# Performance work log

Hardware: AMD Instinct MI355X
Metric: run time of the kernel (lower is better)

The kernel has to match this reference:

```python
import jax, jax.numpy as jnp
import numpy as np

NUM_HEADS = 12


def setup_inputs() -> dict:
    key = jax.random.key(0)
    ks = jax.random.split(key, 10)
    B, N, C = 8, 1024, 768
    H = NUM_HEADS
    return {
        "x": jax.random.normal(ks[0], (B, N, C), dtype=jnp.float32),
        "geometric": jax.random.uniform(ks[1], (B, 1, 1, 1), dtype=jnp.float32),
        "text": jax.random.uniform(ks[2], (B, 1, 1, 1), dtype=jnp.float32),
        "color": jax.random.uniform(ks[3], (B, 1, 1, 1), dtype=jnp.float32),
        "W_qkv": jax.random.normal(ks[4], (C, 3 * C), dtype=jnp.float32) * 0.02,
        "W_proj": jax.random.normal(ks[5], (C, C), dtype=jnp.float32) * 0.02,
        "b_proj": jax.random.normal(ks[6], (C,), dtype=jnp.float32) * 0.02,
        "geo_bias": jax.random.normal(ks[7], (1, H, 1, 1), dtype=jnp.float32) * 0.1,
        "txt_bias": jax.random.normal(ks[8], (1, H, 1, 1), dtype=jnp.float32) * 0.1,
        "col_bias": jax.random.normal(ks[9], (1, H, 1, 1), dtype=jnp.float32) * 0.1,
    }


def reference(x, geometric, text, color, W_qkv, W_proj, b_proj, geo_bias, txt_bias, col_bias):
    B, N, C = x.shape
    H = NUM_HEADS
    Dh = C // H
    scale = Dh ** -0.5
    # qkv: [B, N, 3, H, Dh] -> q,k,v each [B, H, N, Dh]
    qkv = (x @ W_qkv).reshape(B, N, 3, H, Dh)
    q = jnp.transpose(qkv[:, :, 0], (0, 2, 1, 3))
    k = jnp.transpose(qkv[:, :, 1], (0, 2, 1, 3))
    v = jnp.transpose(qkv[:, :, 2], (0, 2, 1, 3))
    # scores [B, H, N, N] with additive per-head logo biases
    attn = jnp.einsum("bhnd,bhmd->bhnm", q, k) * scale
    attn = attn + geo_bias * geometric + txt_bias * text + col_bias * color
    attn = jax.nn.softmax(attn, axis=-1)
    out = jnp.einsum("bhnm,bhmd->bhnd", attn, v)  # [B, H, N, Dh]
    out = jnp.transpose(out, (0, 2, 1, 3)).reshape(B, N, C)
    return out @ W_proj + b_proj
```

## Files before the change

### kernel.cpp

```cpp
#include <hip/hip_runtime.h>
#include <hip/hip_bf16.h>


typedef __bf16 b16x8 __attribute__((ext_vector_type(8)));
typedef float f32x4 __attribute__((ext_vector_type(4)));

__device__ __forceinline__ ushort f2b(float f) {
    union { float f; uint u; } v; v.f = f;
    uint u = v.u;
    u += 0x7fffu + ((u >> 16) & 1u);
    return (ushort)(u >> 16);
}

__device__ __forceinline__ uint packbf(float a, float b) {
    union { float f; uint u; } ua, ub; ua.f = a; ub.f = b;
    return ((ua.u + 0x8000u) >> 16) | ((ub.u + 0x8000u) & 0xffff0000u);
}

__device__ __forceinline__ void async_cp16(const void* g, void* l) {
    __builtin_amdgcn_global_load_lds(
        (const __attribute__((address_space(1))) unsigned int*)g,
        (__attribute__((address_space(3))) unsigned int*)l, 16, 0, 0);
}


__global__ __launch_bounds__(256)
void k_prep(const float* __restrict__ x, ushort* __restrict__ xb,
            const float* __restrict__ Wqkv, ushort* __restrict__ wqkvt,
            const float* __restrict__ Wproj, ushort* __restrict__ wprojt) {
    __shared__ ushort T[64][65];
    const int blk = blockIdx.x;
    const int t   = threadIdx.x;

    if (blk < 6144) {
        const int i = blk * 256 + t;
        const float4 v = reinterpret_cast<const float4*>(x)[i];
        ushort4 o;
        o.x = f2b(v.x); o.y = f2b(v.y); o.z = f2b(v.z); o.w = f2b(v.w);
        reinterpret_cast<ushort4*>(xb)[i] = o;
        return;
    }

    const bool isqkv = (blk < 6576);
    const int idx = isqkv ? (blk - 6144) : (blk - 6576);
    const int Nin = isqkv ? 2304 : 768;
    const float* W  = isqkv ? Wqkv : Wproj;
    ushort* Wt      = isqkv ? wqkvt : wprojt;
    const int k0 = (idx % 12) * 64;
    const int n0 = (idx / 12) * 64;
    const int r  = t >> 4, cg = (t & 15) * 4;
    #pragma unroll
    for (int rr = 0; rr < 64; rr += 16) {
        const float4 v = *reinterpret_cast<const float4*>(&W[(size_t)(k0 + r + rr) * Nin + n0 + cg]);
        T[r + rr][cg + 0] = f2b(v.x); T[r + rr][cg + 1] = f2b(v.y);
        T[r + rr][cg + 2] = f2b(v.z); T[r + rr][cg + 3] = f2b(v.w);
    }
    __syncthreads();
    #pragma unroll
    for (int rr = 0; rr < 64; rr += 16) {
        ushort4 o;
        o.x = T[cg + 0][r + rr]; o.y = T[cg + 1][r + rr];
        o.z = T[cg + 2][r + rr]; o.w = T[cg + 3][r + rr];
        *reinterpret_cast<ushort4*>(&Wt[(size_t)(n0 + r + rr) * 768 + k0 + cg]) = o;
    }
}


template<int MODE>
__global__ __launch_bounds__(256, 4)
void k_gemm(const ushort* __restrict__ A, const ushort* __restrict__ Bt,
            ushort* __restrict__ qo, ushort* __restrict__ ko, ushort* __restrict__ vo,
            float* __restrict__ co, const float* __restrict__ bias,
            int M, int N, int K) {
    __shared__ ushort As[2][128 * 32];
    __shared__ ushort Bs[2][128 * 32];
    const int id   = blockIdx.x;
    const int xcd  = id & 7;
    const int s    = id >> 3;
    const int by   = xcd * 8 + (s & 7);
    const int bx   = s >> 3;
    const int tid  = threadIdx.x;
    const int lane = tid & 63;
    const int w    = tid >> 6;
    const int wm   = w >> 1, wn = w & 1;
    const int m16  = lane & 15, quad = lane >> 4;
    const int mbase = by * 128, nbase = bx * 128;

    f32x4 acc[4][4];
    #pragma unroll
    for (int i = 0; i < 4; i++)
        #pragma unroll
        for (int j = 0; j < 4; j++) acc[i][j] = (f32x4){0.f, 0.f, 0.f, 0.f};

    const int rS = w * 32 + (lane >> 2);
    const int cS = (lane & 3) * 8;
    const int wOff0 = (w * 2 + 0) * 512;
    const int wOff1 = (w * 2 + 1) * 512;
    const ushort* gA0 = &A [(size_t)(mbase + rS)      * K + cS];
    const ushort* gA1 = &A [(size_t)(mbase + rS + 16) * K + cS];
    const ushort* gB0 = &Bt[(size_t)(nbase + rS)      * K + cS];
    const ushort* gB1 = &Bt[(size_t)(nbase + rS + 16) * K + cS];

    async_cp16(gA0, &As[0][wOff0]);
    async_cp16(gA1, &As[0][wOff1]);
    async_cp16(gB0, &Bs[0][wOff0]);
    async_cp16(gB1, &Bs[0][wOff1]);

    for (int kt = 0; kt < K; kt += 32) {
        const int cur = (kt >> 5) & 1, nxt = cur ^ 1;
        __syncthreads();
        if (kt + 32 < K) {
            async_cp16(gA0 + kt + 32, &As[nxt][wOff0]);
            async_cp16(gA1 + kt + 32, &As[nxt][wOff1]);
            async_cp16(gB0 + kt + 32, &Bs[nxt][wOff0]);
            async_cp16(gB1 + kt + 32, &Bs[nxt][wOff1]);
        }

        b16x8 af[4], bf[4];
        #pragma unroll
        for (int i = 0; i < 4; i++)
            af[i] = *reinterpret_cast<const b16x8*>(&As[cur][(wm * 64 + i * 16 + m16) * 32 + quad * 8]);
        #pragma unroll
        for (int j = 0; j < 4; j++)
            bf[j] = *reinterpret_cast<const b16x8*>(&Bs[cur][(wn * 64 + j * 16 + m16) * 32 + quad * 8]);
        #pragma unroll
        for (int i = 0; i < 4; i++)
            #pragma unroll
            for (int j = 0; j < 4; j++)
                acc[i][j] = __builtin_amdgcn_mfma_f32_16x16x32_bf16(bf[j], af[i], acc[i][j], 0, 0, 0);
    }

    #pragma unroll
    for (int j = 0; j < 4; j++) {
        const int f0 = nbase + wn * 64 + j * 16 + quad * 4;
        #pragma unroll
        for (int i = 0; i < 4; i++) {
            const int tok = mbase + wm * 64 + i * 16 + m16;
            const int b = tok >> 10, n = tok & 1023;
            if (MODE == 0) {
                const int sp  = f0 / 768;
                const int rem = f0 - sp * 768;
                const int h   = rem >> 6;
                const int d0  = rem & 63;
                if (sp < 2) {
                    ushort4 pk;
                    pk.x = f2b(acc[i][j][0]); pk.y = f2b(acc[i][j][1]);
                    pk.z = f2b(acc[i][j][2]); pk.w = f2b(acc[i][j][3]);
                    ushort* base = (sp == 0) ? qo : ko;
                    *reinterpret_cast<ushort4*>(
                        &base[((size_t)(b * 12 + h) * 1024 + n) * 64 + d0]) = pk;
                } else {
                    #pragma unroll
                    for (int r = 0; r < 4; r++)
                        vo[((size_t)(b * 12 + h) * 64 + d0 + r) * 1024 + n] =
                            f2b(acc[i][j][r]);
                }
            } else {
                float4 val;
                val.x = acc[i][j][0] + bias[f0 + 0];
                val.y = acc[i][j][1] + bias[f0 + 1];
                val.z = acc[i][j][2] + bias[f0 + 2];
                val.w = acc[i][j][3] + bias[f0 + 3];
                *reinterpret_cast<float4*>(&co[(size_t)tok * N + f0]) = val;
            }
        }
    }
}


#define AP 72

__global__ __launch_bounds__(256)
void k_attn(const ushort* __restrict__ qa, const ushort* __restrict__ ka,
            const ushort* __restrict__ vt, ushort* __restrict__ ao) {
    __shared__ ushort Ks[64 * AP];
    __shared__ ushort Vs[64 * AP];

    const int l    = blockIdx.x;
    const int xcd  = l & 7;
    const int g    = l >> 3;
    const int head = (g % 12) * 8 + xcd;
    const int qsup = g / 12;
    const int tid  = threadIdx.x;
    const int w    = tid >> 6;
    const int lane = tid & 63;
    const int n    = lane & 15;
    const int q    = lane >> 4;

    const ushort* qh = qa + (size_t)head * 65536;
    const ushort* kh = ka + (size_t)head * 65536;
    const ushort* vh = vt + (size_t)head * 65536;
    const int qrow0 = qsup * 128 + w * 32;

    b16x8 bq0[2], bq1[2];
    #pragma unroll
    for (int u = 0; u < 2; u++) {
        bq0[u] = *reinterpret_cast<const b16x8*>(&qh[(qrow0 + u * 16 + n) * 64 + q * 8]);
        bq1[u] = *reinterpret_cast<const b16x8*>(&qh[(qrow0 + u * 16 + n) * 64 + 32 + q * 8]);
    }

    const int kr0 = tid >> 3, kc0 = (tid & 7) * 8;
    const int kr1 = kr0 + 32, kc1 = kc0;

    int4 kg0, kg1, vg0, vg1;
    kg0 = *reinterpret_cast<const int4*>(&kh[(0 + kr0) * 64 + kc0]);
    kg1 = *reinterpret_cast<const int4*>(&kh[(0 + kr1) * 64 + kc1]);
    vg0 = *reinterpret_cast<const int4*>(&vh[kr0 * 1024 + 0 + kc0]);
    vg1 = *reinterpret_cast<const int4*>(&vh[kr1 * 1024 + 0 + kc1]);

    f32x4 o[2][4];
    #pragma unroll
    for (int u = 0; u < 2; u++)
        #pragma unroll
        for (int dt = 0; dt < 4; dt++) o[u][dt] = (f32x4){0, 0, 0, 0};
    float Lacc[2] = {0.f, 0.f};

    const float SC = 0.125f * 1.4426950408889634f;
    const int s0 = ((q & 1) * 2) * 16 + n;
    const int s1 = s0 + 16;
    const bool lowq = (q < 2);

    for (int m0 = 0; m0 < 1024; m0 += 64) {
        *reinterpret_cast<int4*>(&Ks[kr0 * AP + kc0]) = kg0;
        *reinterpret_cast<int4*>(&Ks[kr1 * AP + kc1]) = kg1;
        *reinterpret_cast<int4*>(&Vs[kr0 * AP + kc0]) = vg0;
        *reinterpret_cast<int4*>(&Vs[kr1 * AP + kc1]) = vg1;
        __syncthreads();

        if (m0 + 64 < 1024) {
            kg0 = *reinterpret_cast<const int4*>(&kh[(m0 + 64 + kr0) * 64 + kc0]);
            kg1 = *reinterpret_cast<const int4*>(&kh[(m0 + 64 + kr1) * 64 + kc1]);
            vg0 = *reinterpret_cast<const int4*>(&vh[kr0 * 1024 + m0 + 64 + kc0]);
            vg1 = *reinterpret_cast<const int4*>(&vh[kr1 * 1024 + m0 + 64 + kc1]);
        }

        #pragma unroll
        for (int mc = 0; mc < 2; mc++) {
            b16x8 ka0t[2], ka1t[2];
            #pragma unroll
            for (int t = 0; t < 2; t++) {
                ka0t[t] = *reinterpret_cast<const b16x8*>(&Ks[(mc * 32 + t * 16 + n) * AP + q * 8]);
                ka1t[t] = *reinterpret_cast<const b16x8*>(&Ks[(mc * 32 + t * 16 + n) * AP + 32 + q * 8]);
            }
            f32x4 st[2][2];
            #pragma unroll
            for (int u = 0; u < 2; u++)
                #pragma unroll
                for (int t = 0; t < 2; t++) {
                    st[u][t] = (f32x4){0, 0, 0, 0};
                    st[u][t] = __builtin_amdgcn_mfma_f32_16x16x32_bf16(ka0t[t], bq0[u], st[u][t], 0, 0, 0);
                    st[u][t] = __builtin_amdgcn_mfma_f32_16x16x32_bf16(ka1t[t], bq1[u], st[u][t], 0, 0, 0);
                }

            union { uint4 u4; b16x8 v; } bp[2];
            #pragma unroll
            for (int u = 0; u < 2; u++) {
                float p00 = __builtin_amdgcn_exp2f(st[u][0][0] * SC);
                float p01 = __builtin_amdgcn_exp2f(st[u][0][1] * SC);
                float p02 = __builtin_amdgcn_exp2f(st[u][0][2] * SC);
                float p03 = __builtin_amdgcn_exp2f(st[u][0][3] * SC);
                float p10 = __builtin_amdgcn_exp2f(st[u][1][0] * SC);
                float p11 = __builtin_amdgcn_exp2f(st[u][1][1] * SC);
                float p12 = __builtin_amdgcn_exp2f(st[u][1][2] * SC);
                float p13 = __builtin_amdgcn_exp2f(st[u][1][3] * SC);
                Lacc[u] += ((p00 + p01) + (p02 + p03)) + ((p10 + p11) + (p12 + p13));

                const uint pk00 = packbf(p00, p01), pk01 = packbf(p02, p03);
                const uint pk10 = packbf(p10, p11), pk11 = packbf(p12, p13);

                uint a, b, dw0, dw1, dw2, dw3;
                a = __shfl((int)pk00, s0); b = __shfl((int)pk10, s0); dw0 = lowq ? a : b;
                a = __shfl((int)pk01, s0); b = __shfl((int)pk11, s0); dw1 = lowq ? a : b;
                a = __shfl((int)pk00, s1); b = __shfl((int)pk10, s1); dw2 = lowq ? a : b;
                a = __shfl((int)pk01, s1); b = __shfl((int)pk11, s1); dw3 = lowq ? a : b;
                bp[u].u4 = (uint4){dw0, dw1, dw2, dw3};
            }

            #pragma unroll
            for (int dt = 0; dt < 4; dt++) {
                const b16x8 av = *reinterpret_cast<const b16x8*>(
                    &Vs[(dt * 16 + n) * AP + mc * 32 + q * 8]);
                #pragma unroll
                for (int u = 0; u < 2; u++)
                    o[u][dt] = __builtin_amdgcn_mfma_f32_16x16x32_bf16(av, bp[u].v, o[u][dt], 0, 0, 0);
            }
        }
        __syncthreads();
    }

    const int bb = head / 12, h = head - bb * 12;
    #pragma unroll
    for (int u = 0; u < 2; u++) {
        float L = Lacc[u];
        L += __shfl_xor(L, 16);
        L += __shfl_xor(L, 32);
        const float inv = 1.f / L;
        ushort* dst = ao + ((size_t)(bb * 1024 + qrow0 + u * 16 + n)) * 768 + h * 64 + q * 4;
        #pragma unroll
        for (int dt = 0; dt < 4; dt++) {
            ushort4 pk;
            pk.x = f2b(o[u][dt][0] * inv);
            pk.y = f2b(o[u][dt][1] * inv);
            pk.z = f2b(o[u][dt][2] * inv);
            pk.w = f2b(o[u][dt][3] * inv);
            *reinterpret_cast<ushort4*>(dst + dt * 16) = pk;
        }
    }
}


extern "C" void kernel_launch(void* const* d_in, const int* in_sizes, int n_in,
                              void* d_out, int out_size, void* d_ws, size_t ws_size,
                              hipStream_t stream) {
    (void)in_sizes; (void)n_in; (void)out_size; (void)ws_size;
    const float* x     = (const float*)d_in[0];
    const float* Wqkv  = (const float*)d_in[4];
    const float* Wproj = (const float*)d_in[5];
    const float* bproj = (const float*)d_in[6];
    float* out = (float*)d_out;

    char* ws = (char*)d_ws;
    ushort* xb     = (ushort*)ws; ws += (size_t)8192 * 768 * 2;
    ushort* wqkvt  = (ushort*)ws; ws += (size_t)2304 * 768 * 2;
    ushort* wprojt = (ushort*)ws; ws += (size_t)768  * 768 * 2;
    ushort* qa     = (ushort*)ws; ws += (size_t)96 * 1024 * 64 * 2;
    ushort* ka     = (ushort*)ws; ws += (size_t)96 * 1024 * 64 * 2;
    ushort* vt     = (ushort*)ws; ws += (size_t)96 * 64 * 1024 * 2;
    ushort* ao     = (ushort*)ws; ws += (size_t)8192 * 768 * 2;

    k_prep<<<dim3(6720), dim3(256), 0, stream>>>(x, xb, Wqkv, wqkvt, Wproj, wprojt);
    k_gemm<0><<<dim3(1152), dim3(256), 0, stream>>>(xb, wqkvt, qa, ka, vt,
                                                    nullptr, nullptr, 8192, 2304, 768);
    k_attn<<<dim3(768), dim3(256), 0, stream>>>(qa, ka, vt, ao);
    k_gemm<1><<<dim3(384), dim3(256), 0, stream>>>(ao, wprojt, nullptr, nullptr, nullptr,
                                                   out, bproj, 8192, 768, 768);
}
```

Baseline: 212.6 us.

## Triple-buffer GEMM K-loop and write V transposed via swapped MFMA operands

Moves the GEMM main loop from double to triple buffering with async global-to-LDS copies. Explicit vmcnt waits let two tiles stay in flight while one is consumed, and the loop now needs only one barrier per step. For V-projection blocks the MFMA operands are swapped, so each lane holds 4 consecutive tokens and can write the transposed V output as packed ushort4 stores instead of scattered 2-byte stores. The larger LDS footprint lowers the launch bound to 3 blocks per CU, which reduces occupancy.

```diff
diff --git a/kernel.cpp b/kernel.cpp
--- a/kernel.cpp
+++ b/kernel.cpp
@@ -67,13 +67,13 @@
 
 
 template<int MODE>
-__global__ __launch_bounds__(256, 4)
+__global__ __launch_bounds__(256, 3)
 void k_gemm(const ushort* __restrict__ A, const ushort* __restrict__ Bt,
             ushort* __restrict__ qo, ushort* __restrict__ ko, ushort* __restrict__ vo,
             float* __restrict__ co, const float* __restrict__ bias,
             int M, int N, int K) {
-    __shared__ ushort As[2][128 * 32];
-    __shared__ ushort Bs[2][128 * 32];
+    __shared__ ushort As[3][128 * 32];
+    __shared__ ushort Bs[3][128 * 32];
     const int id   = blockIdx.x;
     const int xcd  = id & 7;
     const int s    = id >> 3;
@@ -85,6 +85,7 @@
     const int wm   = w >> 1, wn = w & 1;
     const int m16  = lane & 15, quad = lane >> 4;
     const int mbase = by * 128, nbase = bx * 128;
+    const bool vblk = (MODE == 0) && (nbase >= 1536);
 
     f32x4 acc[4][4];
     #pragma unroll
@@ -105,15 +106,22 @@
     async_cp16(gA1, &As[0][wOff1]);
     async_cp16(gB0, &Bs[0][wOff0]);
     async_cp16(gB1, &Bs[0][wOff1]);
-
+    async_cp16(gA0 + 32, &As[1][wOff0]);
+    async_cp16(gA1 + 32, &As[1][wOff1]);
+    async_cp16(gB0 + 32, &Bs[1][wOff0]);
+    async_cp16(gB1 + 32, &Bs[1][wOff1]);
+
+    int cur = 0, pre = 2;
     for (int kt = 0; kt < K; kt += 32) {
-        const int cur = (kt >> 5) & 1, nxt = cur ^ 1;
-        __syncthreads();
-        if (kt + 32 < K) {
-            async_cp16(gA0 + kt + 32, &As[nxt][wOff0]);
-            async_cp16(gA1 + kt + 32, &As[nxt][wOff1]);
-            async_cp16(gB0 + kt + 32, &Bs[nxt][wOff0]);
-            async_cp16(gB1 + kt + 32, &Bs[nxt][wOff1]);
+        if (kt + 32 < K) asm volatile("s_waitcnt vmcnt(4)" ::: "memory");
+        else             asm volatile("s_waitcnt vmcnt(0)" ::: "memory");
+        __builtin_amdgcn_s_barrier();
+        if (kt + 64 < K) {
+            const int off = kt + 64;
+            async_cp16(gA0 + off, &As[pre][wOff0]);
+            async_cp16(gA1 + off, &As[pre][wOff1]);
+            async_cp16(gB0 + off, &Bs[pre][wOff0]);
+            async_cp16(gB1 + off, &Bs[pre][wOff1]);
         }
 
         b16x8 af[4], bf[4];
@@ -123,45 +131,68 @@
         #pragma unroll
         for (int j = 0; j < 4; j++)
             bf[j] = *reinterpret_cast<const b16x8*>(&Bs[cur][(wn * 64 + j * 16 + m16) * 32 + quad * 8]);
-        #pragma unroll
-        for (int i = 0; i < 4; i++)
-            #pragma unroll
-            for (int j = 0; j < 4; j++)
-                acc[i][j] = __builtin_amdgcn_mfma_f32_16x16x32_bf16(bf[j], af[i], acc[i][j], 0, 0, 0);
-    }
-
-    #pragma unroll
-    for (int j = 0; j < 4; j++) {
-        const int f0 = nbase + wn * 64 + j * 16 + quad * 4;
-        #pragma unroll
-        for (int i = 0; i < 4; i++) {
-            const int tok = mbase + wm * 64 + i * 16 + m16;
-            const int b = tok >> 10, n = tok & 1023;
-            if (MODE == 0) {
-                const int sp  = f0 / 768;
-                const int rem = f0 - sp * 768;
-                const int h   = rem >> 6;
-                const int d0  = rem & 63;
-                if (sp < 2) {
+        if (vblk) {
+            #pragma unroll
+            for (int i = 0; i < 4; i++)
+                #pragma unroll
+                for (int j = 0; j < 4; j++)
+                    acc[i][j] = __builtin_amdgcn_mfma_f32_16x16x32_bf16(af[i], bf[j], acc[i][j], 0, 0, 0);
+        } else {
+            #pragma unroll
+            for (int i = 0; i < 4; i++)
+                #pragma unroll
+                for (int j = 0; j < 4; j++)
+                    acc[i][j] = __builtin_amdgcn_mfma_f32_16x16x32_bf16(bf[j], af[i], acc[i][j], 0, 0, 0);
+        }
+        cur = (cur == 2) ? 0 : cur + 1;
+        pre = (pre == 2) ? 0 : pre + 1;
+    }
+
+    if (vblk) {
+        #pragma unroll
+        for (int j = 0; j < 4; j++) {
+            const int f   = nbase + wn * 64 + j * 16 + m16;
+            const int rem = f - 1536;
+            const int h   = rem >> 6;
+            const int d0  = rem & 63;
+            #pragma unroll
+            for (int i = 0; i < 4; i++) {
+                const int tok0 = mbase + wm * 64 + i * 16 + quad * 4;
+                const int b = tok0 >> 10, n0 = tok0 & 1023;
+                ushort4 pk;
+                pk.x = f2b(acc[i][j][0]); pk.y = f2b(acc[i][j][1]);
+                pk.z = f2b(acc[i][j][2]); pk.w = f2b(acc[i][j][3]);
+                *reinterpret_cast<ushort4*>(
+                    &vo[((size_t)(b * 12 + h) * 64 + d0) * 1024 + n0]) = pk;
+            }
+        }
+    } else {
+        #pragma unroll
+        for (int j = 0; j < 4; j++) {
+            const int f0 = nbase + wn * 64 + j * 16 + quad * 4;
+            #pragma unroll
+            for (int i = 0; i < 4; i++) {
+                const int tok = mbase + wm * 64 + i * 16 + m16;
+                const int b = tok >> 10, n = tok & 1023;
+                if (MODE == 0) {
+                    const int sp  = (f0 >= 768) ? 1 : 0;
+                    const int rem = f0 - sp * 768;
+                    const int h   = rem >> 6;
+                    const int d0  = rem & 63;
                     ushort4 pk;
                     pk.x = f2b(acc[i][j][0]); pk.y = f2b(acc[i][j][1]);
                     pk.z = f2b(acc[i][j][2]); pk.w = f2b(acc[i][j][3]);
-                    ushort* base = (sp == 0) ? qo : ko;
+                    ushort* base = sp ? ko : qo;
                     *reinterpret_cast<ushort4*>(
                         &base[((size_t)(b * 12 + h) * 1024 + n) * 64 + d0]) = pk;
                 } else {
-                    #pragma unroll
-                    for (int r = 0; r < 4; r++)
-                        vo[((size_t)(b * 12 + h) * 64 + d0 + r) * 1024 + n] =
-                            f2b(acc[i][j][r]);
+                    float4 val;
+                    val.x = acc[i][j][0] + bias[f0 + 0];
+                    val.y = acc[i][j][1] + bias[f0 + 1];
+                    val.z = acc[i][j][2] + bias[f0 + 2];
+                    val.w = acc[i][j][3] + bias[f0 + 3];
+                    *reinterpret_cast<float4*>(&co[(size_t)tok * N + f0]) = val;
                 }
-            } else {
-                float4 val;
-                val.x = acc[i][j][0] + bias[f0 + 0];
-                val.y = acc[i][j][1] + bias[f0 + 1];
-                val.z = acc[i][j][2] + bias[f0 + 2];
-                val.w = acc[i][j][3] + bias[f0 + 3];
-                *reinterpret_cast<float4*>(&co[(size_t)tok * N + f0]) = val;
             }
         }
     }
```

Measured after the change: 245.9 us. +15.7%, slower.
